# Kernel optimization log

Measured on AMD Instinct MI355X. Metric: run time of the kernel, lower is better.

The kernel has to match this reference:

```python
import jax, jax.numpy as jnp
import numpy as np

PULSE_THRESHOLD = 0.01
REAL_W = 1.0
IMAG_W = 1.0
INT_W = 1.0
PHASE_W = 1.0
MSE_W_SUM = REAL_W + IMAG_W + INT_W + PHASE_W


def _hilbert_batch(x):
    # x: [B, N] real. Replicates the module's hilbert(): zero lower half of
    # spectrum, double upper half (N even: bin N/2 kept at 1).
    N = x.shape[-1]
    idx = jnp.arange(N)
    if N % 2 == 0:
        H = jnp.where(idx == N // 2, 1.0, jnp.where(idx > N // 2, 2.0, 0.0))
    else:
        H = jnp.where(idx >= (N + 1) // 2, 2.0, 0.0)
    Xf = jnp.fft.fft(x, axis=-1)
    return jnp.fft.ifft(Xf * H.astype(Xf.dtype), axis=-1)


def _first_last(mask):
    # mask: bool [N]; fallback (0, N-1) when empty, matching torch.nonzero min/max path
    N = mask.shape[0]
    any_m = jnp.any(mask)
    first = jnp.where(any_m, jnp.argmax(mask), 0)
    last = jnp.where(any_m, N - 1 - jnp.argmax(mask[::-1]), N - 1)
    return first, last


def setup_inputs() -> dict:
    key = jax.random.key(0)
    k1, k2, k3, k4 = jax.random.split(key, 4)
    B, N = 512, 8192
    return {
        "prediction": jax.random.normal(k1, (B, N), dtype=jnp.float32),
        "label": jax.random.normal(k2, (B, 2 * N), dtype=jnp.float32),
        "spectrogram": jax.random.uniform(k3, (B, 1, 64, 64), dtype=jnp.float32),
        "header": jax.random.uniform(k4, (B, 5), dtype=jnp.float32),
    }


def reference(prediction, label, spectrogram, header):
    B, N = prediction.shape  # N == half_size
    ana = _hilbert_batch(prediction)              # [B, N] complex64
    pred_real, pred_imag = ana.real, ana.imag
    lab_real = label[:, :N]
    lab_imag = label[:, N:]

    lab_int = lab_real ** 2 + lab_imag ** 2
    pred_int = pred_real ** 2 + pred_imag ** 2
    lab_phase = jnp.arctan2(lab_imag, lab_real)
    pred_phase = jnp.arctan2(pred_imag, pred_real)

    # per-sample significant-region bounds (min of real/imag firsts, max of lasts)
    fr, lr = jax.vmap(_first_last)(jnp.abs(lab_real) > PULSE_THRESHOLD)
    fi, li = jax.vmap(_first_last)(jnp.abs(lab_imag) > PULSE_THRESHOLD)
    first = jnp.minimum(fr, fi)
    last = jnp.maximum(lr, li)
    pos = jnp.arange(N)
    # phase_mask[first:last] = 1 (end-exclusive, as in the torch code)
    phase_mask = ((pos[None, :] >= first[:, None]) & (pos[None, :] < last[:, None])).astype(prediction.dtype)

    mse_real = jnp.mean((pred_real - lab_real) ** 2, axis=-1) * REAL_W
    mse_imag = jnp.mean((pred_imag - lab_imag) ** 2, axis=-1) * IMAG_W
    mse_int = jnp.mean((pred_int - lab_int) ** 2, axis=-1) * INT_W
    mse_phase = jnp.mean(((pred_phase - lab_phase) ** 2) * phase_mask, axis=-1) * PHASE_W
    mse_per = (mse_real + mse_imag + mse_int + mse_phase) / MSE_W_SUM  # [B]

    # The torch loop never resets mse_loss, so sample j contributes (B - j) times.
    coef = (B - jnp.arange(B)).astype(mse_per.dtype)
    loss = jnp.sum(coef * mse_per) / B
    return loss
```

## Files before the change

kernel.cpp:

```cpp
#include <hip/hip_runtime.h>

#define NROWS   512
#define FFT_M   4096
#define THREADS 512
#define PULSE_THR 0.01f

typedef float2 cpx;

__device__ __forceinline__ cpx cadd(cpx a, cpx b){ return make_float2(a.x+b.x, a.y+b.y); }
__device__ __forceinline__ cpx csub(cpx a, cpx b){ return make_float2(a.x-b.x, a.y-b.y); }
__device__ __forceinline__ cpx cmul(cpx a, cpx b){
    return make_float2(fmaf(a.x, b.x, -(a.y*b.y)), fmaf(a.x, b.y, a.y*b.x));
}
__device__ __forceinline__ cpx cmuli(cpx a){ return make_float2(-a.y, a.x); }
__device__ __forceinline__ cpx twf(float rev){
    return make_float2(__builtin_amdgcn_cosf(rev), __builtin_amdgcn_sinf(rev));
}
__device__ __forceinline__ int slotf(int e){ return e ^ ((e >> 4) & 15) ^ ((e >> 8) & 15); }
__device__ __forceinline__ int rev5(int k){
    unsigned r = __brev((unsigned)k) >> 22;
    return (int)(((r & 0x155u) << 1) | ((r & 0x2AAu) >> 1));
}

__device__ __forceinline__ float fast_atan2(float y, float x){
    float ax = fabsf(x), ay = fabsf(y);
    float mx = fmaxf(ax, ay), mn = fminf(ax, ay);
    float a  = mn * __builtin_amdgcn_rcpf(mx);
    if (mx == 0.0f) a = 0.0f;
    float s = a * a;
    float p = fmaf(s, fmaf(s, fmaf(s, fmaf(s, 0.0208351f, -0.085133f),
                                   0.180141f), -0.3302995f), 0.9998660f);
    p = p * a;
    if (ay > ax)   p = 1.57079632679f - p;
    if (x < 0.0f)  p = 3.14159265359f - p;
    return (y < 0.0f) ? -p : p;
}

template<int L>
__device__ __forceinline__ void fwd_stage(cpx* s, int tid){
    constexpr int q = L / 4;
    #pragma unroll
    for (int u = 0; u < 2; ++u){
        int t = tid + THREADS * u;
        int j = t & (q - 1);
        int base = ((t & ~(q - 1)) << 2) + j;
        cpx x0 = s[slotf(base)];
        cpx x1 = s[slotf(base + q)];
        cpx x2 = s[slotf(base + 2*q)];
        cpx x3 = s[slotf(base + 3*q)];
        float rev = -(float)j * (1.0f / (float)L);
        cpx w1 = twf(rev);
        cpx w2 = cmul(w1, w1);
        cpx w3 = cmul(w2, w1);
        cpx a = cadd(x0, x2), b = csub(x0, x2);
        cpx c = cadd(x1, x3), d = csub(x1, x3);
        s[slotf(base)]       = cadd(a, c);
        s[slotf(base + q)]   = cmul(csub(b, cmuli(d)), w1);
        s[slotf(base + 2*q)] = cmul(csub(a, c), w2);
        s[slotf(base + 3*q)] = cmul(cadd(b, cmuli(d)), w3);
    }
}

template<int L>
__device__ __forceinline__ void inv_stage(cpx* s, int tid){
    constexpr int q = L / 4;
    #pragma unroll
    for (int u = 0; u < 2; ++u){
        int t = tid + THREADS * u;
        int j = t & (q - 1);
        int base = ((t & ~(q - 1)) << 2) + j;
        float rev = (float)j * (1.0f / (float)L);
        cpx w1 = twf(rev);
        cpx w2 = cmul(w1, w1);
        cpx w3 = cmul(w2, w1);
        cpx z0 = s[slotf(base)];
        cpx z1 = cmul(s[slotf(base + q)],   w1);
        cpx z2 = cmul(s[slotf(base + 2*q)], w2);
        cpx z3 = cmul(s[slotf(base + 3*q)], w3);
        cpx a = cadd(z0, z2), b = csub(z0, z2);
        cpx c = cadd(z1, z3), d = csub(z1, z3);
        s[slotf(base)]       = cadd(a, c);
        s[slotf(base + q)]   = cadd(b, cmuli(d));
        s[slotf(base + 2*q)] = csub(a, c);
        s[slotf(base + 3*q)] = csub(b, cmuli(d));
    }
}

__device__ __forceinline__ void fwd4(cpx* v){
    cpx a = cadd(v[0], v[2]), b = csub(v[0], v[2]);
    cpx c = cadd(v[1], v[3]), d = csub(v[1], v[3]);
    v[0] = cadd(a, c);
    v[1] = csub(b, cmuli(d));
    v[2] = csub(a, c);
    v[3] = cadd(b, cmuli(d));
}
__device__ __forceinline__ void inv4(cpx* v){
    cpx a = cadd(v[0], v[2]), b = csub(v[0], v[2]);
    cpx c = cadd(v[1], v[3]), d = csub(v[1], v[3]);
    v[0] = cadd(a, c);
    v[1] = cadd(b, cmuli(d));
    v[2] = csub(a, c);
    v[3] = csub(b, cmuli(d));
}

__device__ __forceinline__ void hpair(cpx& Za, cpx& Zb, float krev){
    cpx w  = twf(krev);
    cpx wc = make_float2(w.x, -w.y);
    cpx E  = make_float2(0.5f*(Za.x + Zb.x), 0.5f*(Za.y - Zb.y));
    cpx D  = make_float2(0.5f*(Za.x - Zb.x), 0.5f*(Za.y + Zb.y));
    cpx Ck  = csub(cmul(wc, D), cmul(w, E));
    cpx Ckc = cadd(cmul(w, make_float2(D.x, -D.y)), cmul(wc, make_float2(E.x, -E.y)));
    Za = Ck; Zb = Ckc;
}

__global__ __launch_bounds__(THREADS, 4) void pulse_row_kernel(
    const float* __restrict__ pred,
    const float* __restrict__ label,
    float* __restrict__ mse_per)
{
    __shared__ cpx   sdat[FFT_M];
    __shared__ int   sred[8][4];
    __shared__ float swsum[8];
    __shared__ int   s_first, s_last;
    __shared__ float s_mean;

    const int row  = blockIdx.x;
    const int tid  = threadIdx.x;
    const int lane = tid & 63;
    const int wid  = tid >> 6;

    const float* lab_r = label + (size_t)row * 16384;
    const float* lab_i = lab_r + 8192;

    int minr = 8192, maxr = -1, mini = 8192, maxi = -1;
    const float4* lr4 = (const float4*)lab_r;
    const float4* li4 = (const float4*)lab_i;
    #pragma unroll
    for (int it = 0; it < 4; ++it){
        int idx = tid + THREADS * it;
        float4 a = lr4[idx];
        float4 b = li4[idx];
        int n0 = idx << 2;
        if (fabsf(a.x) > PULSE_THR){ minr = min(minr, n0);   maxr = max(maxr, n0);   }
        if (fabsf(a.y) > PULSE_THR){ minr = min(minr, n0+1); maxr = max(maxr, n0+1); }
        if (fabsf(a.z) > PULSE_THR){ minr = min(minr, n0+2); maxr = max(maxr, n0+2); }
        if (fabsf(a.w) > PULSE_THR){ minr = min(minr, n0+3); maxr = max(maxr, n0+3); }
        if (fabsf(b.x) > PULSE_THR){ mini = min(mini, n0);   maxi = max(maxi, n0);   }
        if (fabsf(b.y) > PULSE_THR){ mini = min(mini, n0+1); maxi = max(maxi, n0+1); }
        if (fabsf(b.z) > PULSE_THR){ mini = min(mini, n0+2); maxi = max(maxi, n0+2); }
        if (fabsf(b.w) > PULSE_THR){ mini = min(mini, n0+3); maxi = max(maxi, n0+3); }
    }
    #pragma unroll
    for (int off = 32; off; off >>= 1){
        minr = min(minr, __shfl_down(minr, off));
        maxr = max(maxr, __shfl_down(maxr, off));
        mini = min(mini, __shfl_down(mini, off));
        maxi = max(maxi, __shfl_down(maxi, off));
    }
    if (lane == 0){ sred[wid][0]=minr; sred[wid][1]=maxr; sred[wid][2]=mini; sred[wid][3]=maxi; }

    const float2* zin = (const float2*)(pred + (size_t)row * 8192);
    cpx zv[8];
    #pragma unroll
    for (int u = 0; u < 8; ++u) zv[u] = zin[tid + THREADS * u];
    #pragma unroll
    for (int b = 0; b < 2; ++b){
        int j = tid + THREADS * b;
        cpx z0 = zv[b], z1 = zv[b+2], z2 = zv[b+4], z3 = zv[b+6];
        cpx a = cadd(z0, z2), bb = csub(z0, z2);
        cpx c = cadd(z1, z3), d = csub(z1, z3);
        float rev = -(float)j * (1.0f / 4096.0f);
        cpx w1 = twf(rev);
        cpx w2 = cmul(w1, w1);
        cpx w3 = cmul(w2, w1);
        sdat[slotf(j)]        = cadd(a, c);
        sdat[slotf(j + 1024)] = cmul(csub(bb, cmuli(d)), w1);
        sdat[slotf(j + 2048)] = cmul(csub(a, c), w2);
        sdat[slotf(j + 3072)] = cmul(cadd(bb, cmuli(d)), w3);
    }
    __syncthreads();

    if (tid == 0){
        int a = 8192, b = -1, c = 8192, d = -1;
        for (int w = 0; w < 8; ++w){
            a = min(a, sred[w][0]); b = max(b, sred[w][1]);
            c = min(c, sred[w][2]); d = max(d, sred[w][3]);
        }
        int fr  = (a == 8192) ? 0 : a;
        int lr_ = (b < 0) ? 8191 : b;
        int fi  = (c == 8192) ? 0 : c;
        int li_ = (d < 0) ? 8191 : d;
        s_first = min(fr, fi);
        s_last  = max(lr_, li_);
    }

    fwd_stage<1024>(sdat, tid); __syncthreads();
    fwd_stage<256 >(sdat, tid); __syncthreads();
    fwd_stage<64  >(sdat, tid); __syncthreads();
    fwd_stage<16  >(sdat, tid); __syncthreads();

    {
        int kA = (tid == 0) ? 0   : tid;
        int kB = (tid == 0) ? 512 : 1024 - tid;
        int pA = rev5(kA) << 2;
        int pB = rev5(kB) << 2;
        cpx va[4], vb[4];
        #pragma unroll
        for (int m = 0; m < 4; ++m){ va[m] = sdat[slotf(pA+m)]; vb[m] = sdat[slotf(pB+m)]; }
        fwd4(va); fwd4(vb);
        if (tid == 0){
            s_mean = (va[0].x + va[0].y) * (1.0f / 8192.0f);
            va[0] = make_float2(0.f, 0.f);
            va[2] = make_float2(va[2].y, -va[2].x);
            hpair(va[1], va[3], 1024.0f / 8192.0f);
            hpair(vb[0], vb[3],  512.0f / 8192.0f);
            hpair(vb[1], vb[2], 1536.0f / 8192.0f);
        } else {
            #pragma unroll
            for (int m = 0; m < 4; ++m){
                float krev = (float)(tid + 1024*m) * (1.0f / 8192.0f);
                hpair(va[m], vb[3-m], krev);
            }
        }
        inv4(va); inv4(vb);
        #pragma unroll
        for (int m = 0; m < 4; ++m){ sdat[slotf(pA+m)] = va[m]; sdat[slotf(pB+m)] = vb[m]; }
    }
    __syncthreads();

    inv_stage<16  >(sdat, tid); __syncthreads();
    inv_stage<64  >(sdat, tid); __syncthreads();
    inv_stage<256 >(sdat, tid); __syncthreads();
    inv_stage<1024>(sdat, tid); __syncthreads();

    const int   first = s_first;
    const int   last  = s_last;
    const float mean  = s_mean;
    const float invM  = 1.0f / 4096.0f;
    const float2* xr2 = (const float2*)(pred + (size_t)row * 8192);
    const float2* lr2 = (const float2*)lab_r;
    const float2* li2 = (const float2*)lab_i;
    float acc = 0.f;
    #pragma unroll
    for (int b = 0; b < 2; ++b){
        int j = tid + THREADS * b;
        float rev = (float)j * (1.0f / 4096.0f);
        cpx w1 = twf(rev);
        cpx w2 = cmul(w1, w1);
        cpx w3 = cmul(w2, w1);
        cpx z0 = sdat[slotf(j)];
        cpx z1 = cmul(sdat[slotf(j + 1024)], w1);
        cpx z2 = cmul(sdat[slotf(j + 2048)], w2);
        cpx z3 = cmul(sdat[slotf(j + 3072)], w3);
        cpx a = cadd(z0, z2), bb = csub(z0, z2);
        cpx c = cadd(z1, z3), d = csub(z1, z3);
        cpx outs[4];
        outs[0] = cadd(a, c);
        outs[1] = cadd(bb, cmuli(d));
        outs[2] = csub(a, c);
        outs[3] = csub(bb, cmuli(d));
        #pragma unroll
        for (int m = 0; m < 4; ++m){
            int t = j + 1024 * m;
            float2 xv  = xr2[t];
            float2 lrv = lr2[t];
            float2 liv = li2[t];
            float pi0 = outs[m].x * invM, pi1 = outs[m].y * invM;
            float pr0 = xv.x - mean,      pr1 = xv.y - mean;
            int n = 2 * t;
            {
                float dr = pr0 - lrv.x, di = pi0 - liv.x;
                acc = fmaf(dr, dr, acc);
                acc = fmaf(di, di, acc);
                float dint = fmaf(pr0, pr0, pi0*pi0) - fmaf(lrv.x, lrv.x, liv.x*liv.x);
                acc = fmaf(dint, dint, acc);
                if (n >= first && n < last){
                    float dph = fast_atan2(pi0, pr0) - fast_atan2(liv.x, lrv.x);
                    acc = fmaf(dph, dph, acc);
                }
            }
            {
                float dr = pr1 - lrv.y, di = pi1 - liv.y;
                acc = fmaf(dr, dr, acc);
                acc = fmaf(di, di, acc);
                float dint = fmaf(pr1, pr1, pi1*pi1) - fmaf(lrv.y, lrv.y, liv.y*liv.y);
                acc = fmaf(dint, dint, acc);
                if (n + 1 >= first && n + 1 < last){
                    float dph = fast_atan2(pi1, pr1) - fast_atan2(liv.y, lrv.y);
                    acc = fmaf(dph, dph, acc);
                }
            }
        }
    }
    #pragma unroll
    for (int off = 32; off; off >>= 1) acc += __shfl_down(acc, off);
    if (lane == 0) swsum[wid] = acc;
    __syncthreads();
    if (tid == 0){
        float t = 0.f;
        for (int w = 0; w < 8; ++w) t += swsum[w];
        mse_per[row] = t * (1.0f / 8192.0f) * 0.25f;
    }
}

__global__ __launch_bounds__(512) void pulse_final_kernel(
    const float* __restrict__ mse_per, float* __restrict__ out)
{
    const int tid = threadIdx.x;
    double v = 0.0;
    if (tid < NROWS) v = (double)(NROWS - tid) * (double)mse_per[tid];
    #pragma unroll
    for (int off = 32; off; off >>= 1) v += __shfl_down(v, off);
    __shared__ double lds[8];
    const int lane = tid & 63, wid = tid >> 6;
    if (lane == 0) lds[wid] = v;
    __syncthreads();
    if (tid == 0){
        double t = 0.0;
        for (int i = 0; i < 8; ++i) t += lds[i];
        out[0] = (float)(t / (double)NROWS);
    }
}

extern "C" void kernel_launch(void* const* d_in, const int* in_sizes, int n_in,
                              void* d_out, int out_size, void* d_ws, size_t ws_size,
                              hipStream_t stream) {
    const float* pred  = (const float*)d_in[0];
    const float* label = (const float*)d_in[1];
    float* mse_per = (float*)d_ws;
    float* out     = (float*)d_out;

    pulse_row_kernel<<<NROWS, THREADS, 0, stream>>>(pred, label, mse_per);
    pulse_final_kernel<<<1, 512, 0, stream>>>(mse_per, out);
}
```

Before: 29.81 us.

## Switch 4096-point FFT from radix-4 to radix-8 stages and reuse loaded prediction

The shared-memory FFT moves from six radix-4 passes to four radix-8 passes, with each thread holding 8 points. This cuts the number of __syncthreads barriers and LDS round-trips on both the forward and inverse paths. The Hilbert pairing step is rebuilt around radix-8 digit-reversed indices and adds one extra barrier between its loads and stores. The final pass takes the real part from the zv registers instead of re-reading the prediction from global memory, at the cost of higher register pressure from the 8-element complex arrays.

```diff
diff --git a/kernel.cpp b/kernel.cpp
--- a/kernel.cpp
+++ b/kernel.cpp
@@ -1,7 +1,6 @@
 #include <hip/hip_runtime.h>
 
 #define NROWS   512
-#define FFT_M   4096
 #define THREADS 512
 #define PULSE_THR 0.01f
 
@@ -17,10 +16,7 @@
     return make_float2(__builtin_amdgcn_cosf(rev), __builtin_amdgcn_sinf(rev));
 }
 __device__ __forceinline__ int slotf(int e){ return e ^ ((e >> 4) & 15) ^ ((e >> 8) & 15); }
-__device__ __forceinline__ int rev5(int k){
-    unsigned r = __brev((unsigned)k) >> 22;
-    return (int)(((r & 0x155u) << 1) | ((r & 0x2AAu) >> 1));
-}
+__device__ __forceinline__ int rev3(int t){ return ((t & 7) << 6) | (t & 0x38) | (t >> 6); }
 
 __device__ __forceinline__ float fast_atan2(float y, float x){
     float ax = fabsf(x), ay = fabsf(y);
@@ -36,81 +32,76 @@
     return (y < 0.0f) ? -p : p;
 }
 
+__device__ __forceinline__ void dft8_fwd(cpx* x){
+    const float S = 0.70710678118654752f;
+    cpx a0=cadd(x[0],x[4]), a1=cadd(x[1],x[5]), a2=cadd(x[2],x[6]), a3=cadd(x[3],x[7]);
+    cpx b0=csub(x[0],x[4]), b1=csub(x[1],x[5]), b2=csub(x[2],x[6]), b3=csub(x[3],x[7]);
+    cpx c0=cadd(a0,a2), c1=csub(a0,a2), c2=cadd(a1,a3), c3=csub(a1,a3);
+    x[0]=cadd(c0,c2);
+    x[4]=csub(c0,c2);
+    x[2]=csub(c1,cmuli(c3));
+    x[6]=cadd(c1,cmuli(c3));
+    cpx t1 = make_float2(S*(b1.x+b1.y), S*(b1.y-b1.x));
+    cpx t2 = make_float2(b2.y, -b2.x);
+    cpx t3 = make_float2(S*(b3.y-b3.x), -S*(b3.x+b3.y));
+    cpx d0=cadd(b0,t2), d1=csub(b0,t2), d2=cadd(t1,t3), d3=csub(t1,t3);
+    x[1]=cadd(d0,d2);
+    x[5]=csub(d0,d2);
+    x[3]=csub(d1,cmuli(d3));
+    x[7]=cadd(d1,cmuli(d3));
+}
+__device__ __forceinline__ void dft8_inv(cpx* x){
+    const float S = 0.70710678118654752f;
+    cpx a0=cadd(x[0],x[4]), a1=cadd(x[1],x[5]), a2=cadd(x[2],x[6]), a3=cadd(x[3],x[7]);
+    cpx b0=csub(x[0],x[4]), b1=csub(x[1],x[5]), b2=csub(x[2],x[6]), b3=csub(x[3],x[7]);
+    cpx c0=cadd(a0,a2), c1=csub(a0,a2), c2=cadd(a1,a3), c3=csub(a1,a3);
+    x[0]=cadd(c0,c2);
+    x[4]=csub(c0,c2);
+    x[2]=cadd(c1,cmuli(c3));
+    x[6]=csub(c1,cmuli(c3));
+    cpx t1 = make_float2(S*(b1.x-b1.y), S*(b1.y+b1.x));
+    cpx t2 = make_float2(-b2.y, b2.x);
+    cpx t3 = make_float2(-S*(b3.x+b3.y), S*(b3.x-b3.y));
+    cpx d0=cadd(b0,t2), d1=csub(b0,t2), d2=cadd(t1,t3), d3=csub(t1,t3);
+    x[1]=cadd(d0,d2);
+    x[5]=csub(d0,d2);
+    x[3]=cadd(d1,cmuli(d3));
+    x[7]=csub(d1,cmuli(d3));
+}
+
 template<int L>
-__device__ __forceinline__ void fwd_stage(cpx* s, int tid){
-    constexpr int q = L / 4;
-    #pragma unroll
-    for (int u = 0; u < 2; ++u){
-        int t = tid + THREADS * u;
-        int j = t & (q - 1);
-        int base = ((t & ~(q - 1)) << 2) + j;
-        cpx x0 = s[slotf(base)];
-        cpx x1 = s[slotf(base + q)];
-        cpx x2 = s[slotf(base + 2*q)];
-        cpx x3 = s[slotf(base + 3*q)];
-        float rev = -(float)j * (1.0f / (float)L);
-        cpx w1 = twf(rev);
-        cpx w2 = cmul(w1, w1);
-        cpx w3 = cmul(w2, w1);
-        cpx a = cadd(x0, x2), b = csub(x0, x2);
-        cpx c = cadd(x1, x3), d = csub(x1, x3);
-        s[slotf(base)]       = cadd(a, c);
-        s[slotf(base + q)]   = cmul(csub(b, cmuli(d)), w1);
-        s[slotf(base + 2*q)] = cmul(csub(a, c), w2);
-        s[slotf(base + 3*q)] = cmul(cadd(b, cmuli(d)), w3);
-    }
-}
-
+__device__ __forceinline__ void fwd_stage8(cpx* sd, int tid){
+    constexpr int q = L / 8;
+    const int j    = tid & (q - 1);
+    const int base = ((tid & ~(q - 1)) << 3) + j;
+    cpx v[8];
+    #pragma unroll
+    for (int m = 0; m < 8; ++m) v[m] = sd[slotf(base + m*q)];
+    dft8_fwd(v);
+    cpx w1 = twf(-(float)j * (1.0f/(float)L));
+    cpx w2 = cmul(w1,w1), w3 = cmul(w2,w1), w4 = cmul(w2,w2);
+    cpx w5 = cmul(w4,w1), w6 = cmul(w3,w3), w7 = cmul(w4,w3);
+    v[1]=cmul(v[1],w1); v[2]=cmul(v[2],w2); v[3]=cmul(v[3],w3);
+    v[4]=cmul(v[4],w4); v[5]=cmul(v[5],w5); v[6]=cmul(v[6],w6); v[7]=cmul(v[7],w7);
+    #pragma unroll
+    for (int m = 0; m < 8; ++m) sd[slotf(base + m*q)] = v[m];
+}
 template<int L>
-__device__ __forceinline__ void inv_stage(cpx* s, int tid){
-    constexpr int q = L / 4;
-    #pragma unroll
-    for (int u = 0; u < 2; ++u){
-        int t = tid + THREADS * u;
-        int j = t & (q - 1);
-        int base = ((t & ~(q - 1)) << 2) + j;
-        float rev = (float)j * (1.0f / (float)L);
-        cpx w1 = twf(rev);
-        cpx w2 = cmul(w1, w1);
-        cpx w3 = cmul(w2, w1);
-        cpx z0 = s[slotf(base)];
-        cpx z1 = cmul(s[slotf(base + q)],   w1);
-        cpx z2 = cmul(s[slotf(base + 2*q)], w2);
-        cpx z3 = cmul(s[slotf(base + 3*q)], w3);
-        cpx a = cadd(z0, z2), b = csub(z0, z2);
-        cpx c = cadd(z1, z3), d = csub(z1, z3);
-        s[slotf(base)]       = cadd(a, c);
-        s[slotf(base + q)]   = cadd(b, cmuli(d));
-        s[slotf(base + 2*q)] = csub(a, c);
-        s[slotf(base + 3*q)] = csub(b, cmuli(d));
-    }
-}
-
-__device__ __forceinline__ void fwd4(cpx* v){
-    cpx a = cadd(v[0], v[2]), b = csub(v[0], v[2]);
-    cpx c = cadd(v[1], v[3]), d = csub(v[1], v[3]);
-    v[0] = cadd(a, c);
-    v[1] = csub(b, cmuli(d));
-    v[2] = csub(a, c);
-    v[3] = cadd(b, cmuli(d));
-}
-__device__ __forceinline__ void inv4(cpx* v){
-    cpx a = cadd(v[0], v[2]), b = csub(v[0], v[2]);
-    cpx c = cadd(v[1], v[3]), d = csub(v[1], v[3]);
-    v[0] = cadd(a, c);
-    v[1] = cadd(b, cmuli(d));
-    v[2] = csub(a, c);
-    v[3] = csub(b, cmuli(d));
-}
-
-__device__ __forceinline__ void hpair(cpx& Za, cpx& Zb, float krev){
-    cpx w  = twf(krev);
-    cpx wc = make_float2(w.x, -w.y);
-    cpx E  = make_float2(0.5f*(Za.x + Zb.x), 0.5f*(Za.y - Zb.y));
-    cpx D  = make_float2(0.5f*(Za.x - Zb.x), 0.5f*(Za.y + Zb.y));
-    cpx Ck  = csub(cmul(wc, D), cmul(w, E));
-    cpx Ckc = cadd(cmul(w, make_float2(D.x, -D.y)), cmul(wc, make_float2(E.x, -E.y)));
-    Za = Ck; Zb = Ckc;
+__device__ __forceinline__ void inv_stage8(cpx* sd, int tid){
+    constexpr int q = L / 8;
+    const int j    = tid & (q - 1);
+    const int base = ((tid & ~(q - 1)) << 3) + j;
+    cpx v[8];
+    #pragma unroll
+    for (int m = 0; m < 8; ++m) v[m] = sd[slotf(base + m*q)];
+    cpx w1 = twf((float)j * (1.0f/(float)L));
+    cpx w2 = cmul(w1,w1), w3 = cmul(w2,w1), w4 = cmul(w2,w2);
+    cpx w5 = cmul(w4,w1), w6 = cmul(w3,w3), w7 = cmul(w4,w3);
+    v[1]=cmul(v[1],w1); v[2]=cmul(v[2],w2); v[3]=cmul(v[3],w3);
+    v[4]=cmul(v[4],w4); v[5]=cmul(v[5],w5); v[6]=cmul(v[6],w6); v[7]=cmul(v[7],w7);
+    dft8_inv(v);
+    #pragma unroll
+    for (int m = 0; m < 8; ++m) sd[slotf(base + m*q)] = v[m];
 }
 
 __global__ __launch_bounds__(THREADS, 4) void pulse_row_kernel(
@@ -118,7 +109,7 @@
     const float* __restrict__ label,
     float* __restrict__ mse_per)
 {
-    __shared__ cpx   sdat[FFT_M];
+    __shared__ cpx   sdat[4096];
     __shared__ int   sred[8][4];
     __shared__ float swsum[8];
     __shared__ int   s_first, s_last;
@@ -163,20 +154,18 @@
     cpx zv[8];
     #pragma unroll
     for (int u = 0; u < 8; ++u) zv[u] = zin[tid + THREADS * u];
-    #pragma unroll
-    for (int b = 0; b < 2; ++b){
-        int j = tid + THREADS * b;
-        cpx z0 = zv[b], z1 = zv[b+2], z2 = zv[b+4], z3 = zv[b+6];
-        cpx a = cadd(z0, z2), bb = csub(z0, z2);
-        cpx c = cadd(z1, z3), d = csub(z1, z3);
-        float rev = -(float)j * (1.0f / 4096.0f);
-        cpx w1 = twf(rev);
-        cpx w2 = cmul(w1, w1);
-        cpx w3 = cmul(w2, w1);
-        sdat[slotf(j)]        = cadd(a, c);
-        sdat[slotf(j + 1024)] = cmul(csub(bb, cmuli(d)), w1);
-        sdat[slotf(j + 2048)] = cmul(csub(a, c), w2);
-        sdat[slotf(j + 3072)] = cmul(cadd(bb, cmuli(d)), w3);
+    {
+        cpx v[8];
+        #pragma unroll
+        for (int m = 0; m < 8; ++m) v[m] = zv[m];
+        dft8_fwd(v);
+        cpx w1 = twf(-(float)tid * (1.0f/4096.0f));
+        cpx w2 = cmul(w1,w1), w3 = cmul(w2,w1), w4 = cmul(w2,w2);
+        cpx w5 = cmul(w4,w1), w6 = cmul(w3,w3), w7 = cmul(w4,w3);
+        v[1]=cmul(v[1],w1); v[2]=cmul(v[2],w2); v[3]=cmul(v[3],w3);
+        v[4]=cmul(v[4],w4); v[5]=cmul(v[5],w5); v[6]=cmul(v[6],w6); v[7]=cmul(v[7],w7);
+        #pragma unroll
+        for (int m = 0; m < 8; ++m) sdat[slotf(tid + 512*m)] = v[m];
     }
     __syncthreads();
 
@@ -194,101 +183,97 @@
         s_last  = max(lr_, li_);
     }
 
-    fwd_stage<1024>(sdat, tid); __syncthreads();
-    fwd_stage<256 >(sdat, tid); __syncthreads();
-    fwd_stage<64  >(sdat, tid); __syncthreads();
-    fwd_stage<16  >(sdat, tid); __syncthreads();
+    fwd_stage8<512>(sdat, tid); __syncthreads();
+    fwd_stage8<64 >(sdat, tid); __syncthreads();
 
     {
-        int kA = (tid == 0) ? 0   : tid;
-        int kB = (tid == 0) ? 512 : 1024 - tid;
-        int pA = rev5(kA) << 2;
-        int pB = rev5(kB) << 2;
-        cpx va[4], vb[4];
-        #pragma unroll
-        for (int m = 0; m < 4; ++m){ va[m] = sdat[slotf(pA+m)]; vb[m] = sdat[slotf(pB+m)]; }
-        fwd4(va); fwd4(vb);
+        const int s  = rev3(tid);
+        const int sp = (512 - s) & 511;
+        const int tp = rev3(sp);
+        cpx va[8], vb[8];
+        #pragma unroll
+        for (int a = 0; a < 8; ++a) va[a] = sdat[slotf(8*tid + a)];
+        #pragma unroll
+        for (int a = 0; a < 8; ++a) vb[a] = sdat[slotf(8*tp  + a)];
+        __syncthreads();
+        dft8_fwd(va);
+        dft8_fwd(vb);
         if (tid == 0){
-            s_mean = (va[0].x + va[0].y) * (1.0f / 8192.0f);
-            va[0] = make_float2(0.f, 0.f);
-            va[2] = make_float2(va[2].y, -va[2].x);
-            hpair(va[1], va[3], 1024.0f / 8192.0f);
-            hpair(vb[0], vb[3],  512.0f / 8192.0f);
-            hpair(vb[1], vb[2], 1536.0f / 8192.0f);
-        } else {
+            s_mean = (va[0].x + va[0].y) * (1.0f/8192.0f);
             #pragma unroll
-            for (int m = 0; m < 4; ++m){
-                float krev = (float)(tid + 1024*m) * (1.0f / 8192.0f);
-                hpair(va[m], vb[3-m], krev);
-            }
-        }
-        inv4(va); inv4(vb);
-        #pragma unroll
-        for (int m = 0; m < 4; ++m){ sdat[slotf(pA+m)] = va[m]; sdat[slotf(pB+m)] = vb[m]; }
+            for (int i = 0; i < 8; ++i) vb[i] = va[(i + 1) & 7];
+        }
+        cpx es = twf((float)s * (1.0f/8192.0f));
+        const float W16c[8] = {1.f, 0.92387953251f, 0.70710678119f, 0.38268343236f,
+                               0.f, -0.38268343236f, -0.70710678119f, -0.92387953251f};
+        const float W16s[8] = {0.f, 0.38268343236f, 0.70710678119f, 0.92387953251f,
+                               1.f, 0.92387953251f, 0.70710678119f, 0.38268343236f};
+        cpx C[8];
+        #pragma unroll
+        for (int a = 0; a < 8; ++a){
+            cpx w  = cmul(make_float2(W16c[a], W16s[a]), es);
+            cpx wc = make_float2(w.x, -w.y);
+            cpx Zb = vb[7 - a];
+            cpx E  = make_float2(0.5f*(va[a].x + Zb.x), 0.5f*(va[a].y - Zb.y));
+            cpx D  = make_float2(0.5f*(va[a].x - Zb.x), 0.5f*(va[a].y + Zb.y));
+            C[a] = csub(cmul(wc, D), cmul(w, E));
+        }
+        if (tid == 0) C[0] = make_float2(0.f, 0.f);
+        dft8_inv(C);
+        #pragma unroll
+        for (int a = 0; a < 8; ++a) sdat[slotf(8*tid + a)] = C[a];
     }
     __syncthreads();
 
-    inv_stage<16  >(sdat, tid); __syncthreads();
-    inv_stage<64  >(sdat, tid); __syncthreads();
-    inv_stage<256 >(sdat, tid); __syncthreads();
-    inv_stage<1024>(sdat, tid); __syncthreads();
+    inv_stage8<64 >(sdat, tid); __syncthreads();
+    inv_stage8<512>(sdat, tid); __syncthreads();
 
     const int   first = s_first;
     const int   last  = s_last;
     const float mean  = s_mean;
-    const float invM  = 1.0f / 4096.0f;
-    const float2* xr2 = (const float2*)(pred + (size_t)row * 8192);
+    const float invM  = 1.0f/4096.0f;
     const float2* lr2 = (const float2*)lab_r;
     const float2* li2 = (const float2*)lab_i;
     float acc = 0.f;
-    #pragma unroll
-    for (int b = 0; b < 2; ++b){
-        int j = tid + THREADS * b;
-        float rev = (float)j * (1.0f / 4096.0f);
-        cpx w1 = twf(rev);
-        cpx w2 = cmul(w1, w1);
-        cpx w3 = cmul(w2, w1);
-        cpx z0 = sdat[slotf(j)];
-        cpx z1 = cmul(sdat[slotf(j + 1024)], w1);
-        cpx z2 = cmul(sdat[slotf(j + 2048)], w2);
-        cpx z3 = cmul(sdat[slotf(j + 3072)], w3);
-        cpx a = cadd(z0, z2), bb = csub(z0, z2);
-        cpx c = cadd(z1, z3), d = csub(z1, z3);
-        cpx outs[4];
-        outs[0] = cadd(a, c);
-        outs[1] = cadd(bb, cmuli(d));
-        outs[2] = csub(a, c);
-        outs[3] = csub(bb, cmuli(d));
-        #pragma unroll
-        for (int m = 0; m < 4; ++m){
-            int t = j + 1024 * m;
-            float2 xv  = xr2[t];
-            float2 lrv = lr2[t];
-            float2 liv = li2[t];
-            float pi0 = outs[m].x * invM, pi1 = outs[m].y * invM;
-            float pr0 = xv.x - mean,      pr1 = xv.y - mean;
-            int n = 2 * t;
-            {
-                float dr = pr0 - lrv.x, di = pi0 - liv.x;
-                acc = fmaf(dr, dr, acc);
-                acc = fmaf(di, di, acc);
-                float dint = fmaf(pr0, pr0, pi0*pi0) - fmaf(lrv.x, lrv.x, liv.x*liv.x);
-                acc = fmaf(dint, dint, acc);
-                if (n >= first && n < last){
-                    float dph = fast_atan2(pi0, pr0) - fast_atan2(liv.x, lrv.x);
-                    acc = fmaf(dph, dph, acc);
-                }
+    cpx y[8];
+    {
+        #pragma unroll
+        for (int m = 0; m < 8; ++m) y[m] = sdat[slotf(tid + 512*m)];
+        cpx w1 = twf((float)tid * (1.0f/4096.0f));
+        cpx w2 = cmul(w1,w1), w3 = cmul(w2,w1), w4 = cmul(w2,w2);
+        cpx w5 = cmul(w4,w1), w6 = cmul(w3,w3), w7 = cmul(w4,w3);
+        y[1]=cmul(y[1],w1); y[2]=cmul(y[2],w2); y[3]=cmul(y[3],w3);
+        y[4]=cmul(y[4],w4); y[5]=cmul(y[5],w5); y[6]=cmul(y[6],w6); y[7]=cmul(y[7],w7);
+        dft8_inv(y);
+    }
+    #pragma unroll
+    for (int m = 0; m < 8; ++m){
+        int tt = tid + 512*m;
+        float2 lrv = lr2[tt];
+        float2 liv = li2[tt];
+        float pi0 = y[m].x * invM, pi1 = y[m].y * invM;
+        float pr0 = zv[m].x - mean, pr1 = zv[m].y - mean;
+        int n = 2 * tt;
+        {
+            float dr = pr0 - lrv.x, di = pi0 - liv.x;
+            acc = fmaf(dr, dr, acc);
+            acc = fmaf(di, di, acc);
+            float dint = fmaf(pr0, pr0, pi0*pi0) - fmaf(lrv.x, lrv.x, liv.x*liv.x);
+            acc = fmaf(dint, dint, acc);
+            if (n >= first && n < last){
+                float dph = fast_atan2(pi0, pr0) - fast_atan2(liv.x, lrv.x);
+                acc = fmaf(dph, dph, acc);
             }
-            {
-                float dr = pr1 - lrv.y, di = pi1 - liv.y;
-                acc = fmaf(dr, dr, acc);
-                acc = fmaf(di, di, acc);
-                float dint = fmaf(pr1, pr1, pi1*pi1) - fmaf(lrv.y, lrv.y, liv.y*liv.y);
-                acc = fmaf(dint, dint, acc);
-                if (n + 1 >= first && n + 1 < last){
-                    float dph = fast_atan2(pi1, pr1) - fast_atan2(liv.y, lrv.y);
-                    acc = fmaf(dph, dph, acc);
-                }
+        }
+        {
+            float dr = pr1 - lrv.y, di = pi1 - liv.y;
+            acc = fmaf(dr, dr, acc);
+            acc = fmaf(di, di, acc);
+            float dint = fmaf(pr1, pr1, pi1*pi1) - fmaf(lrv.y, lrv.y, liv.y*liv.y);
+            acc = fmaf(dint, dint, acc);
+            if (n + 1 >= first && n + 1 < last){
+                float dph = fast_atan2(pi1, pr1) - fast_atan2(liv.y, lrv.y);
+                acc = fmaf(dph, dph, acc);
             }
         }
     }
@@ -299,7 +284,7 @@
     if (tid == 0){
         float t = 0.f;
         for (int w = 0; w < 8; ++w) t += swsum[w];
-        mse_per[row] = t * (1.0f / 8192.0f) * 0.25f;
+        mse_per[row] = t * (1.0f/8192.0f) * 0.25f;
     }
 }
 
```

Result: faster. 28.25 us (-5.2%).

## Use 1024 threads per row, one butterfly per thread, and reuse pred registers

Applied to the files above, without the earlier changes.

Doubles the block to 1024 threads so each FFT stage runs one radix-4 butterfly per thread instead of two. The Hilbert pair step now has every thread compute only its own group's outputs, which needs an extra barrier before the writes. The LDS swizzle changes, and the final loss pass reuses the prediction values held in registers instead of reloading them from global memory. The aim is more parallelism and fewer global loads, at the cost of redundant pair computation and higher register pressure under the new launch bounds.

```diff
diff --git a/kernel.cpp b/kernel.cpp
--- a/kernel.cpp
+++ b/kernel.cpp
@@ -1,8 +1,7 @@
 #include <hip/hip_runtime.h>
 
 #define NROWS   512
-#define FFT_M   4096
-#define THREADS 512
+#define THREADS 1024
 #define PULSE_THR 0.01f
 
 typedef float2 cpx;
@@ -16,7 +15,9 @@
 __device__ __forceinline__ cpx twf(float rev){
     return make_float2(__builtin_amdgcn_cosf(rev), __builtin_amdgcn_sinf(rev));
 }
-__device__ __forceinline__ int slotf(int e){ return e ^ ((e >> 4) & 15) ^ ((e >> 8) & 15); }
+__device__ __forceinline__ int slotf(int e){
+    return e ^ (((e >> 4) & 3) << 2) ^ ((e >> 6) & 3) ^ ((e >> 8) & 15);
+}
 __device__ __forceinline__ int rev5(int k){
     unsigned r = __brev((unsigned)k) >> 22;
     return (int)(((r & 0x155u) << 1) | ((r & 0x2AAu) >> 1));
@@ -37,53 +38,44 @@
 }
 
 template<int L>
-__device__ __forceinline__ void fwd_stage(cpx* s, int tid){
+__device__ __forceinline__ void fwd_stage(cpx* s, int t){
     constexpr int q = L / 4;
-    #pragma unroll
-    for (int u = 0; u < 2; ++u){
-        int t = tid + THREADS * u;
-        int j = t & (q - 1);
-        int base = ((t & ~(q - 1)) << 2) + j;
-        cpx x0 = s[slotf(base)];
-        cpx x1 = s[slotf(base + q)];
-        cpx x2 = s[slotf(base + 2*q)];
-        cpx x3 = s[slotf(base + 3*q)];
-        float rev = -(float)j * (1.0f / (float)L);
-        cpx w1 = twf(rev);
-        cpx w2 = cmul(w1, w1);
-        cpx w3 = cmul(w2, w1);
-        cpx a = cadd(x0, x2), b = csub(x0, x2);
-        cpx c = cadd(x1, x3), d = csub(x1, x3);
-        s[slotf(base)]       = cadd(a, c);
-        s[slotf(base + q)]   = cmul(csub(b, cmuli(d)), w1);
-        s[slotf(base + 2*q)] = cmul(csub(a, c), w2);
-        s[slotf(base + 3*q)] = cmul(cadd(b, cmuli(d)), w3);
-    }
-}
-
+    const int j    = t & (q - 1);
+    const int base = ((t & ~(q - 1)) << 2) + j;
+    cpx x0 = s[slotf(base)];
+    cpx x1 = s[slotf(base + q)];
+    cpx x2 = s[slotf(base + 2*q)];
+    cpx x3 = s[slotf(base + 3*q)];
+    float rev = -(float)j * (1.0f / (float)L);
+    cpx w1 = twf(rev);
+    cpx w2 = cmul(w1, w1);
+    cpx w3 = cmul(w2, w1);
+    cpx a = cadd(x0, x2), b = csub(x0, x2);
+    cpx c = cadd(x1, x3), d = csub(x1, x3);
+    s[slotf(base)]       = cadd(a, c);
+    s[slotf(base + q)]   = cmul(csub(b, cmuli(d)), w1);
+    s[slotf(base + 2*q)] = cmul(csub(a, c), w2);
+    s[slotf(base + 3*q)] = cmul(cadd(b, cmuli(d)), w3);
+}
 template<int L>
-__device__ __forceinline__ void inv_stage(cpx* s, int tid){
+__device__ __forceinline__ void inv_stage(cpx* s, int t){
     constexpr int q = L / 4;
-    #pragma unroll
-    for (int u = 0; u < 2; ++u){
-        int t = tid + THREADS * u;
-        int j = t & (q - 1);
-        int base = ((t & ~(q - 1)) << 2) + j;
-        float rev = (float)j * (1.0f / (float)L);
-        cpx w1 = twf(rev);
-        cpx w2 = cmul(w1, w1);
-        cpx w3 = cmul(w2, w1);
-        cpx z0 = s[slotf(base)];
-        cpx z1 = cmul(s[slotf(base + q)],   w1);
-        cpx z2 = cmul(s[slotf(base + 2*q)], w2);
-        cpx z3 = cmul(s[slotf(base + 3*q)], w3);
-        cpx a = cadd(z0, z2), b = csub(z0, z2);
-        cpx c = cadd(z1, z3), d = csub(z1, z3);
-        s[slotf(base)]       = cadd(a, c);
-        s[slotf(base + q)]   = cadd(b, cmuli(d));
-        s[slotf(base + 2*q)] = csub(a, c);
-        s[slotf(base + 3*q)] = csub(b, cmuli(d));
-    }
+    const int j    = t & (q - 1);
+    const int base = ((t & ~(q - 1)) << 2) + j;
+    float rev = (float)j * (1.0f / (float)L);
+    cpx w1 = twf(rev);
+    cpx w2 = cmul(w1, w1);
+    cpx w3 = cmul(w2, w1);
+    cpx z0 = s[slotf(base)];
+    cpx z1 = cmul(s[slotf(base + q)],   w1);
+    cpx z2 = cmul(s[slotf(base + 2*q)], w2);
+    cpx z3 = cmul(s[slotf(base + 3*q)], w3);
+    cpx a = cadd(z0, z2), b = csub(z0, z2);
+    cpx c = cadd(z1, z3), d = csub(z1, z3);
+    s[slotf(base)]       = cadd(a, c);
+    s[slotf(base + q)]   = cadd(b, cmuli(d));
+    s[slotf(base + 2*q)] = csub(a, c);
+    s[slotf(base + 3*q)] = csub(b, cmuli(d));
 }
 
 __device__ __forceinline__ void fwd4(cpx* v){
@@ -103,24 +95,14 @@
     v[3] = csub(b, cmuli(d));
 }
 
-__device__ __forceinline__ void hpair(cpx& Za, cpx& Zb, float krev){
-    cpx w  = twf(krev);
-    cpx wc = make_float2(w.x, -w.y);
-    cpx E  = make_float2(0.5f*(Za.x + Zb.x), 0.5f*(Za.y - Zb.y));
-    cpx D  = make_float2(0.5f*(Za.x - Zb.x), 0.5f*(Za.y + Zb.y));
-    cpx Ck  = csub(cmul(wc, D), cmul(w, E));
-    cpx Ckc = cadd(cmul(w, make_float2(D.x, -D.y)), cmul(wc, make_float2(E.x, -E.y)));
-    Za = Ck; Zb = Ckc;
-}
-
-__global__ __launch_bounds__(THREADS, 4) void pulse_row_kernel(
+__global__ __launch_bounds__(THREADS, 8) void pulse_row_kernel(
     const float* __restrict__ pred,
     const float* __restrict__ label,
     float* __restrict__ mse_per)
 {
-    __shared__ cpx   sdat[FFT_M];
-    __shared__ int   sred[8][4];
-    __shared__ float swsum[8];
+    __shared__ cpx   sdat[4096];
+    __shared__ int   sred[16][4];
+    __shared__ float swsum[16];
     __shared__ int   s_first, s_last;
     __shared__ float s_mean;
 
@@ -136,7 +118,7 @@
     const float4* lr4 = (const float4*)lab_r;
     const float4* li4 = (const float4*)lab_i;
     #pragma unroll
-    for (int it = 0; it < 4; ++it){
+    for (int it = 0; it < 2; ++it){
         int idx = tid + THREADS * it;
         float4 a = lr4[idx];
         float4 b = li4[idx];
@@ -160,29 +142,25 @@
     if (lane == 0){ sred[wid][0]=minr; sred[wid][1]=maxr; sred[wid][2]=mini; sred[wid][3]=maxi; }
 
     const float2* zin = (const float2*)(pred + (size_t)row * 8192);
-    cpx zv[8];
-    #pragma unroll
-    for (int u = 0; u < 8; ++u) zv[u] = zin[tid + THREADS * u];
-    #pragma unroll
-    for (int b = 0; b < 2; ++b){
-        int j = tid + THREADS * b;
-        cpx z0 = zv[b], z1 = zv[b+2], z2 = zv[b+4], z3 = zv[b+6];
-        cpx a = cadd(z0, z2), bb = csub(z0, z2);
-        cpx c = cadd(z1, z3), d = csub(z1, z3);
-        float rev = -(float)j * (1.0f / 4096.0f);
-        cpx w1 = twf(rev);
+    cpx zv[4];
+    #pragma unroll
+    for (int u = 0; u < 4; ++u) zv[u] = zin[tid + THREADS * u];
+    {
+        cpx a = cadd(zv[0], zv[2]), b = csub(zv[0], zv[2]);
+        cpx c = cadd(zv[1], zv[3]), d = csub(zv[1], zv[3]);
+        cpx w1 = twf(-(float)tid * (1.0f/4096.0f));
         cpx w2 = cmul(w1, w1);
         cpx w3 = cmul(w2, w1);
-        sdat[slotf(j)]        = cadd(a, c);
-        sdat[slotf(j + 1024)] = cmul(csub(bb, cmuli(d)), w1);
-        sdat[slotf(j + 2048)] = cmul(csub(a, c), w2);
-        sdat[slotf(j + 3072)] = cmul(cadd(bb, cmuli(d)), w3);
+        sdat[slotf(tid)]        = cadd(a, c);
+        sdat[slotf(tid + 1024)] = cmul(csub(b, cmuli(d)), w1);
+        sdat[slotf(tid + 2048)] = cmul(csub(a, c), w2);
+        sdat[slotf(tid + 3072)] = cmul(cadd(b, cmuli(d)), w3);
     }
     __syncthreads();
 
     if (tid == 0){
         int a = 8192, b = -1, c = 8192, d = -1;
-        for (int w = 0; w < 8; ++w){
+        for (int w = 0; w < 16; ++w){
             a = min(a, sred[w][0]); b = max(b, sred[w][1]);
             c = min(c, sred[w][2]); d = max(d, sred[w][3]);
         }
@@ -200,31 +178,43 @@
     fwd_stage<16  >(sdat, tid); __syncthreads();
 
     {
-        int kA = (tid == 0) ? 0   : tid;
-        int kB = (tid == 0) ? 512 : 1024 - tid;
-        int pA = rev5(kA) << 2;
-        int pB = rev5(kB) << 2;
+        const int s  = tid;
+        const int sp = (1024 - s) & 1023;
+        const int gA = rev5(s);
+        const int gB = rev5(sp);
         cpx va[4], vb[4];
         #pragma unroll
-        for (int m = 0; m < 4; ++m){ va[m] = sdat[slotf(pA+m)]; vb[m] = sdat[slotf(pB+m)]; }
-        fwd4(va); fwd4(vb);
+        for (int m = 0; m < 4; ++m) va[m] = sdat[slotf(4*gA + m)];
+        #pragma unroll
+        for (int m = 0; m < 4; ++m) vb[m] = sdat[slotf(4*gB + m)];
+        __syncthreads();
+        fwd4(va);
+        fwd4(vb);
         if (tid == 0){
-            s_mean = (va[0].x + va[0].y) * (1.0f / 8192.0f);
-            va[0] = make_float2(0.f, 0.f);
-            va[2] = make_float2(va[2].y, -va[2].x);
-            hpair(va[1], va[3], 1024.0f / 8192.0f);
-            hpair(vb[0], vb[3],  512.0f / 8192.0f);
-            hpair(vb[1], vb[2], 1536.0f / 8192.0f);
-        } else {
-            #pragma unroll
-            for (int m = 0; m < 4; ++m){
-                float krev = (float)(tid + 1024*m) * (1.0f / 8192.0f);
-                hpair(va[m], vb[3-m], krev);
-            }
-        }
-        inv4(va); inv4(vb);
+            s_mean = (va[0].x + va[0].y) * (1.0f/8192.0f);
+            cpx t0 = va[0];
+            vb[0] = va[1]; vb[1] = va[2]; vb[2] = va[3]; vb[3] = t0;
+        }
+        cpx es = twf((float)s * (1.0f/8192.0f));
+        const float S2 = 0.70710678118654752f;
+        cpx C[4];
         #pragma unroll
-        for (int m = 0; m < 4; ++m){ sdat[slotf(pA+m)] = va[m]; sdat[slotf(pB+m)] = vb[m]; }
+        for (int a = 0; a < 4; ++a){
+            cpx w;
+            if      (a == 0) w = es;
+            else if (a == 1) w = cmul(make_float2( S2, S2), es);
+            else if (a == 2) w = cmuli(es);
+            else             w = cmul(make_float2(-S2, S2), es);
+            cpx wc = make_float2(w.x, -w.y);
+            cpx Zb = vb[3 - a];
+            cpx E  = make_float2(0.5f*(va[a].x + Zb.x), 0.5f*(va[a].y - Zb.y));
+            cpx D  = make_float2(0.5f*(va[a].x - Zb.x), 0.5f*(va[a].y + Zb.y));
+            C[a] = csub(cmul(wc, D), cmul(w, E));
+        }
+        if (tid == 0) C[0] = make_float2(0.f, 0.f);
+        inv4(C);
+        #pragma unroll
+        for (int m = 0; m < 4; ++m) sdat[slotf(4*gA + m)] = C[m];
     }
     __syncthreads();
 
@@ -236,59 +226,54 @@
     const int   first = s_first;
     const int   last  = s_last;
     const float mean  = s_mean;
-    const float invM  = 1.0f / 4096.0f;
-    const float2* xr2 = (const float2*)(pred + (size_t)row * 8192);
+    const float invM  = 1.0f/4096.0f;
     const float2* lr2 = (const float2*)lab_r;
     const float2* li2 = (const float2*)lab_i;
     float acc = 0.f;
-    #pragma unroll
-    for (int b = 0; b < 2; ++b){
-        int j = tid + THREADS * b;
-        float rev = (float)j * (1.0f / 4096.0f);
-        cpx w1 = twf(rev);
+    cpx y[4];
+    {
+        cpx z0 = sdat[slotf(tid)];
+        cpx w1 = twf((float)tid * (1.0f/4096.0f));
         cpx w2 = cmul(w1, w1);
         cpx w3 = cmul(w2, w1);
-        cpx z0 = sdat[slotf(j)];
-        cpx z1 = cmul(sdat[slotf(j + 1024)], w1);
-        cpx z2 = cmul(sdat[slotf(j + 2048)], w2);
-        cpx z3 = cmul(sdat[slotf(j + 3072)], w3);
-        cpx a = cadd(z0, z2), bb = csub(z0, z2);
+        cpx z1 = cmul(sdat[slotf(tid + 1024)], w1);
+        cpx z2 = cmul(sdat[slotf(tid + 2048)], w2);
+        cpx z3 = cmul(sdat[slotf(tid + 3072)], w3);
+        cpx a = cadd(z0, z2), b = csub(z0, z2);
         cpx c = cadd(z1, z3), d = csub(z1, z3);
-        cpx outs[4];
-        outs[0] = cadd(a, c);
-        outs[1] = cadd(bb, cmuli(d));
-        outs[2] = csub(a, c);
-        outs[3] = csub(bb, cmuli(d));
-        #pragma unroll
-        for (int m = 0; m < 4; ++m){
-            int t = j + 1024 * m;
-            float2 xv  = xr2[t];
-            float2 lrv = lr2[t];
-            float2 liv = li2[t];
-            float pi0 = outs[m].x * invM, pi1 = outs[m].y * invM;
-            float pr0 = xv.x - mean,      pr1 = xv.y - mean;
-            int n = 2 * t;
-            {
-                float dr = pr0 - lrv.x, di = pi0 - liv.x;
-                acc = fmaf(dr, dr, acc);
-                acc = fmaf(di, di, acc);
-                float dint = fmaf(pr0, pr0, pi0*pi0) - fmaf(lrv.x, lrv.x, liv.x*liv.x);
-                acc = fmaf(dint, dint, acc);
-                if (n >= first && n < last){
-                    float dph = fast_atan2(pi0, pr0) - fast_atan2(liv.x, lrv.x);
-                    acc = fmaf(dph, dph, acc);
-                }
+        y[0] = cadd(a, c);
+        y[1] = cadd(b, cmuli(d));
+        y[2] = csub(a, c);
+        y[3] = csub(b, cmuli(d));
+    }
+    #pragma unroll
+    for (int m = 0; m < 4; ++m){
+        int tt = tid + 1024*m;
+        float2 lrv = lr2[tt];
+        float2 liv = li2[tt];
+        float pi0 = y[m].x * invM, pi1 = y[m].y * invM;
+        float pr0 = zv[m].x - mean, pr1 = zv[m].y - mean;
+        int n = 2 * tt;
+        {
+            float dr = pr0 - lrv.x, di = pi0 - liv.x;
+            acc = fmaf(dr, dr, acc);
+            acc = fmaf(di, di, acc);
+            float dint = fmaf(pr0, pr0, pi0*pi0) - fmaf(lrv.x, lrv.x, liv.x*liv.x);
+            acc = fmaf(dint, dint, acc);
+            if (n >= first && n < last){
+                float dph = fast_atan2(pi0, pr0) - fast_atan2(liv.x, lrv.x);
+                acc = fmaf(dph, dph, acc);
             }
-            {
-                float dr = pr1 - lrv.y, di = pi1 - liv.y;
-                acc = fmaf(dr, dr, acc);
-                acc = fmaf(di, di, acc);
-                float dint = fmaf(pr1, pr1, pi1*pi1) - fmaf(lrv.y, lrv.y, liv.y*liv.y);
-                acc = fmaf(dint, dint, acc);
-                if (n + 1 >= first && n + 1 < last){
-                    float dph = fast_atan2(pi1, pr1) - fast_atan2(liv.y, lrv.y);
-                    acc = fmaf(dph, dph, acc);
-                }
+        }
+        {
+            float dr = pr1 - lrv.y, di = pi1 - liv.y;
+            acc = fmaf(dr, dr, acc);
+            acc = fmaf(di, di, acc);
+            float dint = fmaf(pr1, pr1, pi1*pi1) - fmaf(lrv.y, lrv.y, liv.y*liv.y);
+            acc = fmaf(dint, dint, acc);
+            if (n + 1 >= first && n + 1 < last){
+                float dph = fast_atan2(pi1, pr1) - fast_atan2(liv.y, lrv.y);
+                acc = fmaf(dph, dph, acc);
             }
         }
     }
@@ -298,8 +283,8 @@
     __syncthreads();
     if (tid == 0){
         float t = 0.f;
-        for (int w = 0; w < 8; ++w) t += swsum[w];
-        mse_per[row] = t * (1.0f / 8192.0f) * 0.25f;
+        for (int w = 0; w < 16; ++w) t += swsum[w];
+        mse_per[row] = t * (1.0f/8192.0f) * 0.25f;
     }
 }
 
```

Result: slower. 33.02 us (+10.8%).
